# Kernel tuning notes

Hardware: AMD Instinct MI355X
Metric: run time of the kernel (lower is better)

The kernel has to match this reference:

```python
import jax, jax.numpy as jnp
import numpy as np

K = 3
STRIDE = 1
PADDING = 1
INVALID = -1.0


def _unfold(x, k, stride, padding, fill):
    # x: [B, C, H, W] -> patches [B, C, k, k, P] matching torch F.unfold ordering
    x = jnp.pad(x, ((0, 0), (0, 0), (padding, padding), (padding, padding)),
                constant_values=fill)
    # feature dim ordered channel-major (C, kh, kw), same as torch unfold
    p = jax.lax.conv_general_dilated_patches(x, (k, k), (stride, stride), 'VALID')
    b, _, ho, wo = p.shape
    c = x.shape[1]
    return p.reshape(b, c, k, k, ho * wo), ho, wo


def setup_inputs() -> dict:
    key = jax.random.key(0)
    k1, k2, k3, k4 = jax.random.split(key, 4)
    B, C, H, W = 8, 64, 128, 128
    OC = 64
    inp = jax.random.normal(k1, (B, C, H, W), dtype=jnp.float32)
    mask = jax.random.randint(k2, (B, H, W), 0, 4).astype(jnp.float32)
    conv = jax.random.normal(k3, (OC, C, K, K), dtype=jnp.float32) * 0.05
    bias = jax.random.normal(k4, (OC,), dtype=jnp.float32) * 0.05
    return {"inp": inp, "mask": mask, "conv": conv, "bias": bias}


def reference(inp, mask, conv, bias):
    k, stride, padding = K, STRIDE, PADDING
    b, c, h_in, w_in = inp.shape
    oc = conv.shape[0]
    center = (k - 1) // 2

    inp_patched, ho, wo = _unfold(inp, k, stride, padding, INVALID)       # [B,C,k,k,P]
    mask_patched, _, _ = _unfold(mask[:, None], k, stride, padding, INVALID)  # [B,1,k,k,P]
    mask_patched = mask_patched[:, 0]                                      # [B,k,k,P]

    center_val = mask_patched[:, center:center + 1, center:center + 1, :]  # [B,1,1,P]
    mask_eq = (mask_patched == center_val).astype(inp.dtype)               # [B,k,k,P]

    masked_input = inp_patched * mask_eq[:, None]                          # [B,C,k,k,P]
    m_norm = (k * k) / jnp.clip(mask_eq.reshape(b, k * k, -1).sum(axis=1), 1e-8)  # [B,P]

    masked_input = masked_input.reshape(b, c, k * k, -1)                   # [B,C,kk,P]
    w = conv.reshape(oc, c, k * k)                                         # [O,C,kk]
    out = jnp.einsum('bcxp,ocx->bop', masked_input, w)                     # [B,O,P]
    out = out * m_norm[:, None, :]
    out = out.reshape(b, oc, ho, wo)
    out = out + bias[None, :, None, None]

    mask_out = mask_patched[:, center, center, :].reshape(b, 1, ho, wo)
    return out, mask_out
```

## Files before the change

kernel.cpp:

```cpp
#include <hip/hip_runtime.h>
#include <stdint.h>

#define HW   128
#define CIN  64
#define OCN  64
#define NB   8

typedef __attribute__((ext_vector_type(8)))  short short8;
typedef __attribute__((ext_vector_type(16))) float floatx16;
typedef unsigned long long u64;

union F8 { short8 s; u64 u[2]; uint32_t d[4]; uint4 q; };

static __device__ __forceinline__ ushort f2bf(float f) {
    uint32_t u = __float_as_uint(f);
    uint32_t r = (u + 0x7FFFu + ((u >> 16) & 1u)) >> 16;
    return (ushort)r;
}

__global__ void wprep_kernel(const float* __restrict__ conv, ushort* __restrict__ wb) {
    int idx  = blockIdx.x * 256 + threadIdx.x;
    int j    = idx & 7;
    int lane = (idx >> 3) & 63;
    int m    = (idx >> 9) & 1;
    int ks   = (idx >> 10) & 3;
    int t    = idx >> 12;
    int oc   = m * 32 + (lane & 31);
    int c    = ks * 16 + (lane >> 5) * 8 + j;
    wb[idx] = f2bf(conv[(oc * 64 + c) * 9 + t]);
}

#define XS_CSTR 68
#define XS_ROW  (HW * XS_CSTR)
#define LDS_BYTES 71936

__global__ __launch_bounds__(256, 2)
void iconv_main(const float* __restrict__ inp, const float* __restrict__ mask,
                const ushort* __restrict__ wb, const float* __restrict__ bias,
                float* __restrict__ out)
{
    extern __shared__ char smem[];
    ushort* Xs = (ushort*)smem;
    float*  Ms = (float*)(smem + 69632);
    float*  Bb = (float*)(smem + 71680);

    const int tid  = threadIdx.x;
    const int bb   = blockIdx.x >> 6;
    const int y0   = (blockIdx.x & 63) << 1;
    const int lane = tid & 63;
    const int l31  = lane & 31;
    const int lh   = lane >> 5;
    const int w    = tid >> 6;
    const int yloc = w >> 1;
    const int xw   = (w & 1) * 64;
    const int y    = y0 + yloc;

    const ushort* aBase = wb + lane * 8;
    uint4 a_cur[8];
    #pragma unroll
    for (int f = 0; f < 8; ++f)
        a_cur[f] = *(const uint4*)(aBase + f * 512);

    {
        const int cp = tid & 31;
        const int xq = (tid >> 5) * 16;
        const float* base0 = inp + ((size_t)(bb * CIN + 2 * cp) * HW) * HW;
        #pragma unroll
        for (int rr = 0; rr < 4; ++rr) {
            int gy = y0 - 1 + rr;
            if (gy >= 0 && gy < HW) {
                const float4* q0 = (const float4*)(base0 + (size_t)gy * HW + xq);
                const float4* q1 = (const float4*)(base0 + (size_t)HW * HW + (size_t)gy * HW + xq);
                float4 v0[4], v1[4];
                #pragma unroll
                for (int i = 0; i < 4; ++i) { v0[i] = q0[i]; v1[i] = q1[i]; }
                ushort* xrow = Xs + rr * XS_ROW + xq * XS_CSTR + 2 * cp;
                const float* f0 = (const float*)v0;
                const float* f1 = (const float*)v1;
                #pragma unroll
                for (int i = 0; i < 16; ++i) {
                    uint32_t p = (uint32_t)f2bf(f0[i]) | ((uint32_t)f2bf(f1[i]) << 16);
                    *(uint32_t*)(xrow + i * XS_CSTR) = p;
                }
            }
        }
    }
    {
        int rr = tid >> 6, x0 = (tid & 63) * 2;
        int gy = y0 - 1 + rr;
        if (gy >= 0 && gy < HW) {
            float2 v = *(const float2*)(mask + ((size_t)bb * HW + gy) * HW + x0);
            Ms[rr * HW + x0]     = v.x;
            Ms[rr * HW + x0 + 1] = v.y;
        }
    }
    if (tid < OCN) Bb[tid] = bias[tid];

    __syncthreads();

    {
        int yy = tid >> 7, x = tid & 127;
        float mv = Ms[(1 + yy) * HW + x];
        __builtin_nontemporal_store(
            mv, out + (size_t)NB * OCN * HW * HW + ((size_t)bb * HW + y0 + yy) * HW + x);
    }

    uint32_t sel[9][2];
    float norm0, norm1;
    {
        int cnt0 = 0, cnt1 = 0;
        int xq0 = xw + l31, xq1 = xw + 32 + l31;
        float m00 = Ms[(1 + yloc) * HW + xq0];
        float m01 = Ms[(1 + yloc) * HW + xq1];
        #pragma unroll
        for (int t = 0; t < 9; ++t) {
            int dy = t / 3 - 1, dx = t % 3 - 1;
            int ny = y + dy;
            bool vy = (ny >= 0) && (ny < HW);
            int rbase = (1 + yloc + dy) * HW;
            {
                int nx = xq0 + dx;
                bool ok = vy && (nx >= 0) && (nx < HW);
                int nxc = nx < 0 ? 0 : (nx > HW - 1 ? HW - 1 : nx);
                bool eq = ok && (Ms[rbase + nxc] == m00);
                sel[t][0] = eq ? 0xFFFFFFFFu : 0u;
                cnt0 += eq ? 1 : 0;
            }
            {
                int nx = xq1 + dx;
                bool ok = vy && (nx >= 0) && (nx < HW);
                int nxc = nx < 0 ? 0 : (nx > HW - 1 ? HW - 1 : nx);
                bool eq = ok && (Ms[rbase + nxc] == m01);
                sel[t][1] = eq ? 0xFFFFFFFFu : 0u;
                cnt1 += eq ? 1 : 0;
            }
        }
        norm0 = 9.0f / (float)cnt0;
        norm1 = 9.0f / (float)cnt1;
    }

    floatx16 acc00 = {0,0,0,0,0,0,0,0,0,0,0,0,0,0,0,0};
    floatx16 acc01 = {0,0,0,0,0,0,0,0,0,0,0,0,0,0,0,0};
    floatx16 acc10 = {0,0,0,0,0,0,0,0,0,0,0,0,0,0,0,0};
    floatx16 acc11 = {0,0,0,0,0,0,0,0,0,0,0,0,0,0,0,0};

    #pragma unroll
    for (int t = 0; t < 9; ++t) {
        uint4 a_nxt[8];
        if (t < 8) {
            #pragma unroll
            for (int f = 0; f < 8; ++f)
                a_nxt[f] = *(const uint4*)(aBase + ((t + 1) * 8 + f) * 512);
        }

        const int dy = t / 3 - 1, dx = t % 3 - 1;
        const int rrB = 1 + yloc + dy;
        int xa = xw + l31 + dx;
        int xb0c = xa < 0 ? 0 : (xa > HW - 1 ? HW - 1 : xa);
        int xa1 = xa + 32;
        int xb1c = xa1 < 0 ? 0 : (xa1 > HW - 1 ? HW - 1 : xa1);
        const ushort* B0p = Xs + rrB * XS_ROW + xb0c * XS_CSTR + lh * 8;
        const ushort* B1p = Xs + rrB * XS_ROW + xb1c * XS_CSTR + lh * 8;
        const uint32_t s0 = sel[t][0], s1 = sel[t][1];

        #pragma unroll
        for (int ks = 0; ks < 4; ++ks) {
            F8 a0, a1, b0, b1;
            a0.q = a_cur[ks * 2 + 0];
            a1.q = a_cur[ks * 2 + 1];
            b0.u[0] = *(const u64*)(B0p + ks * 16);
            b0.u[1] = *(const u64*)(B0p + ks * 16 + 4);
            b1.u[0] = *(const u64*)(B1p + ks * 16);
            b1.u[1] = *(const u64*)(B1p + ks * 16 + 4);
            b0.d[0] &= s0; b0.d[1] &= s0; b0.d[2] &= s0; b0.d[3] &= s0;
            b1.d[0] &= s1; b1.d[1] &= s1; b1.d[2] &= s1; b1.d[3] &= s1;
            acc00 = __builtin_amdgcn_mfma_f32_32x32x16_bf16(a0.s, b0.s, acc00, 0, 0, 0);
            acc01 = __builtin_amdgcn_mfma_f32_32x32x16_bf16(a0.s, b1.s, acc01, 0, 0, 0);
            acc10 = __builtin_amdgcn_mfma_f32_32x32x16_bf16(a1.s, b0.s, acc10, 0, 0, 0);
            acc11 = __builtin_amdgcn_mfma_f32_32x32x16_bf16(a1.s, b1.s, acc11, 0, 0, 0);
        }

        #pragma unroll
        for (int f = 0; f < 8; ++f)
            if (t < 8) a_cur[f] = a_nxt[f];
    }

    float* outp = out + (size_t)bb * OCN * HW * HW + (size_t)y * HW;
    #pragma unroll
    for (int mt = 0; mt < 2; ++mt) {
        #pragma unroll
        for (int nt = 0; nt < 2; ++nt) {
            floatx16 a = (mt == 0) ? (nt == 0 ? acc00 : acc01)
                                   : (nt == 0 ? acc10 : acc11);
            float nm = (nt == 0) ? norm0 : norm1;
            int x = xw + nt * 32 + l31;
            #pragma unroll
            for (int r = 0; r < 16; ++r) {
                int oc = mt * 32 + (r & 3) + 8 * (r >> 2) + 4 * lh;
                __builtin_nontemporal_store(a[r] * nm + Bb[oc],
                                            outp + (size_t)oc * (HW * HW) + x);
            }
        }
    }
}

extern "C" void kernel_launch(void* const* d_in, const int* in_sizes, int n_in,
                              void* d_out, int out_size, void* d_ws, size_t ws_size,
                              hipStream_t stream) {
    (void)in_sizes; (void)n_in; (void)out_size; (void)ws_size;
    const float* inp  = (const float*)d_in[0];
    const float* mask = (const float*)d_in[1];
    const float* conv = (const float*)d_in[2];
    const float* bias = (const float*)d_in[3];
    float* out = (float*)d_out;
    ushort* wb = (ushort*)d_ws;

    hipFuncSetAttribute((const void*)iconv_main,
                        hipFuncAttributeMaxDynamicSharedMemorySize, LDS_BYTES);

    wprep_kernel<<<144, 256, 0, stream>>>(conv, wb);
    iconv_main<<<NB * (HW / 2), 256, LDS_BYTES, stream>>>(inp, mask, wb, bias, out);
}
```

Measured before the change: 103.6 us.

## Split row tiles into half-width blocks with static LDS and higher occupancy

Each block now covers two rows by 64 columns instead of two full rows, so the grid doubles and the staged input tile shrinks to 72 columns with a 4-column halo. LDS per block drops to about 40KB, which allows a launch bound of four blocks per CU. A swizzled block index groups neighbouring tiles. Weights are loaded from global memory inside the MFMA loop rather than prefetched into registers, and each wave now holds two accumulators instead of four. The cost is more halo loads, more redundant weight fetches per output, and less MFMA work per wave.

```diff
diff --git a/kernel.cpp b/kernel.cpp
--- a/kernel.cpp
+++ b/kernel.cpp
@@ -31,54 +31,58 @@
 }
 
 #define XS_CSTR 68
-#define XS_ROW  (HW * XS_CSTR)
-#define LDS_BYTES 71936
+#define XS_COLS 72
+#define XS_ROW  (XS_COLS * XS_CSTR)
 
-__global__ __launch_bounds__(256, 2)
+__global__ __launch_bounds__(256, 4)
 void iconv_main(const float* __restrict__ inp, const float* __restrict__ mask,
                 const ushort* __restrict__ wb, const float* __restrict__ bias,
                 float* __restrict__ out)
 {
-    extern __shared__ char smem[];
-    ushort* Xs = (ushort*)smem;
-    float*  Ms = (float*)(smem + 69632);
-    float*  Bb = (float*)(smem + 71680);
+    __shared__ ushort Xs[4 * XS_ROW];
+    __shared__ float  Ms[4 * XS_COLS];
+    __shared__ float  Bb[OCN];
 
     const int tid  = threadIdx.x;
-    const int bb   = blockIdx.x >> 6;
-    const int y0   = (blockIdx.x & 63) << 1;
+
+    const int d   = blockIdx.x;
+    const int Lg  = (d & 7) * 128 + (d >> 3);
+    const int bb  = Lg >> 7;
+    const int rb  = Lg & 127;
+    const int y0  = (rb >> 1) << 1;
+    const int xh  = rb & 1;
+    const int xbase = xh * 64;
+
     const int lane = tid & 63;
     const int l31  = lane & 31;
     const int lh   = lane >> 5;
     const int w    = tid >> 6;
     const int yloc = w >> 1;
-    const int xw   = (w & 1) * 64;
+    const int xq   = (w & 1) * 32;
     const int y    = y0 + yloc;
-
-    const ushort* aBase = wb + lane * 8;
-    uint4 a_cur[8];
-    #pragma unroll
-    for (int f = 0; f < 8; ++f)
-        a_cur[f] = *(const uint4*)(aBase + f * 512);
+    const int xl   = xq + l31;
+    const int xg   = xbase + xl;
 
     {
         const int cp = tid & 31;
-        const int xq = (tid >> 5) * 16;
+        const int gq = tid >> 5;
         const float* base0 = inp + ((size_t)(bb * CIN + 2 * cp) * HW) * HW;
         #pragma unroll
-        for (int rr = 0; rr < 4; ++rr) {
+        for (int k = 0; k < 9; ++k) {
+            int task = gq + k * 8;
+            int rr = task / 18;
+            int G  = task - rr * 18;
             int gy = y0 - 1 + rr;
-            if (gy >= 0 && gy < HW) {
-                const float4* q0 = (const float4*)(base0 + (size_t)gy * HW + xq);
-                const float4* q1 = (const float4*)(base0 + (size_t)HW * HW + (size_t)gy * HW + xq);
-                float4 v0[4], v1[4];
+            int gx0 = xbase - 4 + 4 * G;
+            if (gy >= 0 && gy < HW && gx0 >= 0 && gx0 <= HW - 4) {
+                const float* r0 = base0 + (size_t)gy * HW + gx0;
+                float4 v0 = *(const float4*)(r0);
+                float4 v1 = *(const float4*)(r0 + (size_t)HW * HW);
+                const float* f0 = (const float*)&v0;
+                const float* f1 = (const float*)&v1;
+                ushort* xrow = Xs + rr * XS_ROW + 4 * G * XS_CSTR + 2 * cp;
                 #pragma unroll
-                for (int i = 0; i < 4; ++i) { v0[i] = q0[i]; v1[i] = q1[i]; }
-                ushort* xrow = Xs + rr * XS_ROW + xq * XS_CSTR + 2 * cp;
-                const float* f0 = (const float*)v0;
-                const float* f1 = (const float*)v1;
-                #pragma unroll
-                for (int i = 0; i < 16; ++i) {
+                for (int i = 0; i < 4; ++i) {
                     uint32_t p = (uint32_t)f2bf(f0[i]) | ((uint32_t)f2bf(f1[i]) << 16);
                     *(uint32_t*)(xrow + i * XS_CSTR) = p;
                 }
@@ -86,120 +90,85 @@
         }
     }
     {
-        int rr = tid >> 6, x0 = (tid & 63) * 2;
+        int rr = tid >> 6, l2 = tid & 63;
         int gy = y0 - 1 + rr;
         if (gy >= 0 && gy < HW) {
-            float2 v = *(const float2*)(mask + ((size_t)bb * HW + gy) * HW + x0);
-            Ms[rr * HW + x0]     = v.x;
-            Ms[rr * HW + x0 + 1] = v.y;
+            const float* mrow = mask + ((size_t)bb * HW + gy) * HW;
+            #pragma unroll
+            for (int kk = 0; kk < 2; ++kk) {
+                int L = 2 * l2 + kk;
+                if (L < XS_COLS) {
+                    int gx = xbase - 4 + L;
+                    int gxc = gx < 0 ? 0 : (gx > HW - 1 ? HW - 1 : gx);
+                    Ms[rr * XS_COLS + L] = mrow[gxc];
+                }
+            }
         }
     }
     if (tid < OCN) Bb[tid] = bias[tid];
 
     __syncthreads();
 
-    {
-        int yy = tid >> 7, x = tid & 127;
-        float mv = Ms[(1 + yy) * HW + x];
+    if (tid < 128) {
+        int yy = tid >> 6, xlm = tid & 63;
+        float mv = Ms[(1 + yy) * XS_COLS + xlm + 4];
         __builtin_nontemporal_store(
-            mv, out + (size_t)NB * OCN * HW * HW + ((size_t)bb * HW + y0 + yy) * HW + x);
+            mv, out + (size_t)NB * OCN * HW * HW + ((size_t)bb * HW + y0 + yy) * HW + xbase + xlm);
     }
 
-    uint32_t sel[9][2];
-    float norm0, norm1;
+    uint32_t sel[9];
+    float norm;
     {
-        int cnt0 = 0, cnt1 = 0;
-        int xq0 = xw + l31, xq1 = xw + 32 + l31;
-        float m00 = Ms[(1 + yloc) * HW + xq0];
-        float m01 = Ms[(1 + yloc) * HW + xq1];
+        int cnt = 0;
+        int xl4 = xl + 4;
+        float m0 = Ms[(1 + yloc) * XS_COLS + xl4];
         #pragma unroll
         for (int t = 0; t < 9; ++t) {
             int dy = t / 3 - 1, dx = t % 3 - 1;
             int ny = y + dy;
             bool vy = (ny >= 0) && (ny < HW);
-            int rbase = (1 + yloc + dy) * HW;
-            {
-                int nx = xq0 + dx;
-                bool ok = vy && (nx >= 0) && (nx < HW);
-                int nxc = nx < 0 ? 0 : (nx > HW - 1 ? HW - 1 : nx);
-                bool eq = ok && (Ms[rbase + nxc] == m00);
-                sel[t][0] = eq ? 0xFFFFFFFFu : 0u;
-                cnt0 += eq ? 1 : 0;
-            }
-            {
-                int nx = xq1 + dx;
-                bool ok = vy && (nx >= 0) && (nx < HW);
-                int nxc = nx < 0 ? 0 : (nx > HW - 1 ? HW - 1 : nx);
-                bool eq = ok && (Ms[rbase + nxc] == m01);
-                sel[t][1] = eq ? 0xFFFFFFFFu : 0u;
-                cnt1 += eq ? 1 : 0;
-            }
+            int gxn = xg + dx;
+            bool ok = vy && (gxn >= 0) && (gxn < HW);
+            bool eq = ok && (Ms[(1 + yloc + dy) * XS_COLS + xl4 + dx] == m0);
+            sel[t] = eq ? 0xFFFFFFFFu : 0u;
+            cnt += eq ? 1 : 0;
         }
-        norm0 = 9.0f / (float)cnt0;
-        norm1 = 9.0f / (float)cnt1;
+        norm = 9.0f / (float)cnt;
     }
 
-    floatx16 acc00 = {0,0,0,0,0,0,0,0,0,0,0,0,0,0,0,0};
-    floatx16 acc01 = {0,0,0,0,0,0,0,0,0,0,0,0,0,0,0,0};
-    floatx16 acc10 = {0,0,0,0,0,0,0,0,0,0,0,0,0,0,0,0};
-    floatx16 acc11 = {0,0,0,0,0,0,0,0,0,0,0,0,0,0,0,0};
+    floatx16 acc0 = {0,0,0,0,0,0,0,0,0,0,0,0,0,0,0,0};
+    floatx16 acc1 = {0,0,0,0,0,0,0,0,0,0,0,0,0,0,0,0};
 
+    const ushort* aBase = wb + lane * 8;
     #pragma unroll
     for (int t = 0; t < 9; ++t) {
-        uint4 a_nxt[8];
-        if (t < 8) {
-            #pragma unroll
-            for (int f = 0; f < 8; ++f)
-                a_nxt[f] = *(const uint4*)(aBase + ((t + 1) * 8 + f) * 512);
-        }
-
         const int dy = t / 3 - 1, dx = t % 3 - 1;
         const int rrB = 1 + yloc + dy;
-        int xa = xw + l31 + dx;
-        int xb0c = xa < 0 ? 0 : (xa > HW - 1 ? HW - 1 : xa);
-        int xa1 = xa + 32;
-        int xb1c = xa1 < 0 ? 0 : (xa1 > HW - 1 ? HW - 1 : xa1);
-        const ushort* B0p = Xs + rrB * XS_ROW + xb0c * XS_CSTR + lh * 8;
-        const ushort* B1p = Xs + rrB * XS_ROW + xb1c * XS_CSTR + lh * 8;
-        const uint32_t s0 = sel[t][0], s1 = sel[t][1];
+        const ushort* Bp = Xs + rrB * XS_ROW + (xl + dx + 4) * XS_CSTR + lh * 8;
+        const uint32_t s0 = sel[t];
 
         #pragma unroll
         for (int ks = 0; ks < 4; ++ks) {
-            F8 a0, a1, b0, b1;
-            a0.q = a_cur[ks * 2 + 0];
-            a1.q = a_cur[ks * 2 + 1];
-            b0.u[0] = *(const u64*)(B0p + ks * 16);
-            b0.u[1] = *(const u64*)(B0p + ks * 16 + 4);
-            b1.u[0] = *(const u64*)(B1p + ks * 16);
-            b1.u[1] = *(const u64*)(B1p + ks * 16 + 4);
+            F8 a0, a1, b0;
+            a0.q = *(const uint4*)(aBase + (t * 8 + ks * 2 + 0) * 512);
+            a1.q = *(const uint4*)(aBase + (t * 8 + ks * 2 + 1) * 512);
+            b0.u[0] = *(const u64*)(Bp + ks * 16);
+            b0.u[1] = *(const u64*)(Bp + ks * 16 + 4);
             b0.d[0] &= s0; b0.d[1] &= s0; b0.d[2] &= s0; b0.d[3] &= s0;
-            b1.d[0] &= s1; b1.d[1] &= s1; b1.d[2] &= s1; b1.d[3] &= s1;
-            acc00 = __builtin_amdgcn_mfma_f32_32x32x16_bf16(a0.s, b0.s, acc00, 0, 0, 0);
-            acc01 = __builtin_amdgcn_mfma_f32_32x32x16_bf16(a0.s, b1.s, acc01, 0, 0, 0);
-            acc10 = __builtin_amdgcn_mfma_f32_32x32x16_bf16(a1.s, b0.s, acc10, 0, 0, 0);
-            acc11 = __builtin_amdgcn_mfma_f32_32x32x16_bf16(a1.s, b1.s, acc11, 0, 0, 0);
+            acc0 = __builtin_amdgcn_mfma_f32_32x32x16_bf16(a0.s, b0.s, acc0, 0, 0, 0);
+            acc1 = __builtin_amdgcn_mfma_f32_32x32x16_bf16(a1.s, b0.s, acc1, 0, 0, 0);
         }
-
-        #pragma unroll
-        for (int f = 0; f < 8; ++f)
-            if (t < 8) a_cur[f] = a_nxt[f];
     }
 
-    float* outp = out + (size_t)bb * OCN * HW * HW + (size_t)y * HW;
+    float* outp = out + (size_t)bb * OCN * HW * HW + (size_t)y * HW + xg;
     #pragma unroll
     for (int mt = 0; mt < 2; ++mt) {
+        floatx16 a = (mt == 0) ? acc0 : acc1;
         #pragma unroll
-        for (int nt = 0; nt < 2; ++nt) {
-            floatx16 a = (mt == 0) ? (nt == 0 ? acc00 : acc01)
-                                   : (nt == 0 ? acc10 : acc11);
-            float nm = (nt == 0) ? norm0 : norm1;
-            int x = xw + nt * 32 + l31;
-            #pragma unroll
-            for (int r = 0; r < 16; ++r) {
-                int oc = mt * 32 + (r & 3) + 8 * (r >> 2) + 4 * lh;
-                __builtin_nontemporal_store(a[r] * nm + Bb[oc],
-                                            outp + (size_t)oc * (HW * HW) + x);
-            }
+        for (int r = 0; r < 16; ++r) {
+            int oc = mt * 32 + (r & 3) + 8 * (r >> 2) + 4 * lh;
+            __builtin_nontemporal_store(a[r] * norm + Bb[oc],
+                                        outp + (size_t)oc * (HW * HW));
         }
     }
 }
@@ -215,9 +184,6 @@
     float* out = (float*)d_out;
     ushort* wb = (ushort*)d_ws;
 
-    hipFuncSetAttribute((const void*)iconv_main,
-                        hipFuncAttributeMaxDynamicSharedMemorySize, LDS_BYTES);
-
     wprep_kernel<<<144, 256, 0, stream>>>(conv, wb);
-    iconv_main<<<NB * (HW / 2), 256, LDS_BYTES, stream>>>(inp, mask, wb, bias, out);
+    iconv_main<<<NB * (HW / 2) * 2, 256, 0, stream>>>(inp, mask, wb, bias, out);
 }
```

Measured after the change: 113.6 us. +9.6%, slower.
